# Optimization experiments

Measured on AMD Instinct MI355X. Metric: run time of the kernel, lower is better.

The kernel has to match this reference:

```python
import jax, jax.numpy as jnp
import numpy as np

B, N, A, M, D = 64, 128, 64, 128, 64  # batch, in_caps, in_dim, out_caps, out_dim
SCALE = 1.0 / np.sqrt(D).astype(np.float32)
W_INIT = np.sqrt(M / (A * N)).astype(np.float32)


def setup_inputs() -> dict:
    key = jax.random.key(0)
    k1, k2, k3, k4, k5 = jax.random.split(key, 5)
    return {
        "input": jax.random.normal(k1, (B, N, A), dtype=jnp.float32),
        "current_act": jax.random.uniform(k2, (B, N), dtype=jnp.float32),
        "next_capsule_value": jax.random.normal(k3, (B, M, D), dtype=jnp.float32),
        "next_act": jax.random.uniform(k4, (B, M), dtype=jnp.float32),
        "w": W_INIT * jax.random.normal(k5, (N, A, M, D), dtype=jnp.float32),
        "num_iter": 1,
    }


def reference(input, current_act, next_capsule_value, next_act, w, num_iter):
    # Per-(input-capsule, output-capsule) votes: bna,namd->bnmd (shared by both einsums)
    votes = jnp.einsum('bna,namd->bnmd', input, w)
    # Routing logits: agreement between votes and current output poses
    logits = jnp.einsum('bnmd,bmd->bnm', votes, next_capsule_value) * SCALE
    qk = jax.nn.softmax(logits, axis=2)
    # Modulate by next-layer activations and renormalize over output capsules
    qk = qk * next_act[:, None, :]
    qk = qk / (jnp.sum(qk, axis=2, keepdims=True) + 1e-10)
    # Weighted aggregation of votes, gated by input-capsule activations
    ncv = jnp.einsum('bnm,bnmd,bn->bmd', qk, votes, current_act)
    # act_type == 'ONES'; dropout rate 0.0 (identity); nonlinear_act is identity
    na = jnp.ones(ncv.shape[:2], dtype=ncv.dtype)
    return ncv, na, qk
```

## Files before the change

kernel.cpp:

```cpp
#include <hip/hip_runtime.h>

typedef __attribute__((ext_vector_type(8))) short bf16x8;
typedef __attribute__((ext_vector_type(4))) float f32x4;

constexpr int Bq = 64, Nq = 128, Aq = 64, Mq = 128, Dq = 64;
constexpr int MD = Mq * Dq;
constexpr int NM = Nq * Mq;
constexpr int NA = Nq * Aq;
constexpr int NCV_SZ = Bq * MD;
constexpr int NA_SZ  = Bq * Mq;
constexpr float SCALE = 0.125f;

__device__ __forceinline__ unsigned short f2b(float f) {
  unsigned u = __float_as_uint(f);
  return (unsigned short)((u + 0x7fffu + ((u >> 16) & 1u)) >> 16);
}
__device__ __forceinline__ unsigned cvt2(float lo, float hi) {
  return ((unsigned)f2b(hi) << 16) | (unsigned)f2b(lo);
}
__device__ __forceinline__ bf16x8 pack8(const float* v) {
  union { unsigned u[4]; bf16x8 b; } x;
  x.u[0] = cvt2(v[0], v[1]); x.u[1] = cvt2(v[2], v[3]);
  x.u[2] = cvt2(v[4], v[5]); x.u[3] = cvt2(v[6], v[7]);
  return x.b;
}
__device__ __forceinline__ void dma16(const float* g, float* l) {
  __builtin_amdgcn_global_load_lds(
      (const __attribute__((address_space(1))) unsigned*)g,
      (__attribute__((address_space(3))) unsigned*)l, 16, 0, 0);
}

__global__ __launch_bounds__(256) void k0_init(float* __restrict__ out) {
  int i = blockIdx.x * 256 + threadIdx.x;
  if (i < NCV_SZ) out[i] = 0.0f;
  else if (i < NCV_SZ + NA_SZ) out[i] = 1.0f;
}

__global__ __launch_bounds__(512, 4) void k1_logits(
    const float* __restrict__ input, const float* __restrict__ ncvin,
    const float* __restrict__ wgt, float* __restrict__ logits) {
  const int mc = blockIdx.x;
  const int n0 = blockIdx.y * 8;
  const int t = threadIdx.x;
  const int w8 = t >> 6, l = t & 63;
  const int wv_m = w8 & 3, wv_b = w8 >> 2;
  const int lr = l & 15, g = l >> 4;
  const int m = mc * 4 + wv_m;
  __shared__ float Wf[2][32 * 256];

  float cnv[2][4][4];
#pragma unroll
  for (int i = 0; i < 2; ++i)
#pragma unroll
    for (int j = 0; j < 4; ++j)
#pragma unroll
      for (int r = 0; r < 4; ++r)
        cnv[i][j][r] = ncvin[(size_t)(32 * wv_b + 16 * i + 4 * g + r) * MD + m * Dq + 16 * j + lr];

  auto stage = [&](int h) {
    const int hh = 15 - h;
    const int nn = n0 + (hh >> 1);
    const int ks = (hh & 1) * 32;
    float* dst = &Wf[h & 1][0];
#pragma unroll
    for (int rr = 0; rr < 4; ++rr) {
      const int al = w8 * 4 + rr;
      const char* gs = (const char*)(wgt + (size_t)(nn * Aq + ks + al) * MD + mc * 256)
                       + ((l * 16) ^ (((al >> 3) & 1) << 6));
      dma16((const float*)gs, dst + al * 256);
    }
  };
  stage(0);
  f32x4 acc[2][4];

  for (int h = 0; h < 16; ++h) {
    const int hh = 15 - h;
    const int nn = n0 + (hh >> 1);
    const int ks = (hh & 1) * 32;

    float av[2][8];
#pragma unroll
    for (int i = 0; i < 2; ++i) {
      const float* ap = input + (size_t)(32 * wv_b + 16 * i + lr) * NA + nn * Aq + ks + g * 8;
      *(float4*)&av[i][0] = *(const float4*)ap;
      *(float4*)&av[i][4] = *(const float4*)(ap + 4);
    }
    __builtin_amdgcn_sched_barrier(0);

    if (h < 15) {
      stage(h + 1);
      asm volatile("s_waitcnt vmcnt(4)" ::: "memory");
    } else {
      asm volatile("s_waitcnt vmcnt(0)" ::: "memory");
    }
    __builtin_amdgcn_s_barrier();

    if ((h & 1) == 0) {
#pragma unroll
      for (int i = 0; i < 2; ++i)
#pragma unroll
        for (int j = 0; j < 4; ++j) acc[i][j] = (f32x4)(0.0f);
    }

    bf16x8 af[2];
#pragma unroll
    for (int i = 0; i < 2; ++i) af[i] = pack8(av[i]);

    const float* bufp = &Wf[h & 1][0];
#pragma unroll
    for (int j = 0; j < 4; ++j) {
      const int cx = (64 * wv_m + 16 * j + lr) ^ ((g & 1) << 4);
      float bv[8];
#pragma unroll
      for (int e = 0; e < 8; ++e) bv[e] = bufp[(g * 8 + e) * 256 + cx];
      bf16x8 bf = pack8(bv);
#pragma unroll
      for (int i = 0; i < 2; ++i)
        acc[i][j] = __builtin_amdgcn_mfma_f32_16x16x32_bf16(af[i], bf, acc[i][j], 0, 0, 0);
    }
    __builtin_amdgcn_s_barrier();

    if (h & 1) {
      float lp[2][4];
#pragma unroll
      for (int i = 0; i < 2; ++i)
#pragma unroll
        for (int r = 0; r < 4; ++r) lp[i][r] = 0.0f;
#pragma unroll
      for (int i = 0; i < 2; ++i)
#pragma unroll
        for (int j = 0; j < 4; ++j)
#pragma unroll
          for (int r = 0; r < 4; ++r)
            lp[i][r] = fmaf(acc[i][j][r], cnv[i][j][r], lp[i][r]);
#pragma unroll
      for (int off = 1; off < 16; off <<= 1)
#pragma unroll
        for (int i = 0; i < 2; ++i)
#pragma unroll
          for (int r = 0; r < 4; ++r) lp[i][r] += __shfl_xor(lp[i][r], off);
      float ov = lp[0][0];
#pragma unroll
      for (int i = 0; i < 2; ++i)
#pragma unroll
        for (int r = 0; r < 4; ++r)
          ov = (lr == i * 4 + r) ? lp[i][r] : ov;
      if (lr < 8) {
        const int b = 32 * wv_b + 16 * (lr >> 2) + 4 * g + (lr & 3);
        logits[(size_t)b * NM + (size_t)nn * Mq + m] = SCALE * ov;
      }
    }
  }
}

__global__ __launch_bounds__(256) void k2_softmax(
    const float* __restrict__ next_act, float* __restrict__ qk) {
  const int row  = blockIdx.x * 4 + (threadIdx.x >> 6);
  const int lane = threadIdx.x & 63;
  const int b = row >> 7;
  float* p = qk + (size_t)row * Mq;
  float x0 = p[lane], x1 = p[lane + 64];
  float mx = fmaxf(x0, x1);
#pragma unroll
  for (int off = 32; off; off >>= 1) mx = fmaxf(mx, __shfl_xor(mx, off));
  float e0 = __expf(x0 - mx), e1 = __expf(x1 - mx);
  float s = e0 + e1;
#pragma unroll
  for (int off = 32; off; off >>= 1) s += __shfl_xor(s, off);
  float a0 = next_act[b * Mq + lane], a1 = next_act[b * Mq + lane + 64];
  float t0 = (e0 / s) * a0, t1 = (e1 / s) * a1;
  float s2 = t0 + t1;
#pragma unroll
  for (int off = 32; off; off >>= 1) s2 += __shfl_xor(s2, off);
  s2 += 1e-10f;
  p[lane]      = t0 / s2;
  p[lane + 64] = t1 / s2;
}

__global__ __launch_bounds__(512, 4) void k3_aggregate(
    const float* __restrict__ input, const float* __restrict__ cur_act,
    const float* __restrict__ wgt, const float* __restrict__ qk,
    float* __restrict__ ncv) {
  const int mc = blockIdx.x;
  const int n0 = blockIdx.y * 8;
  const int t = threadIdx.x;
  const int w8 = t >> 6, l = t & 63;
  const int wv_m = w8 & 3, wv_b = w8 >> 2;
  const int lr = l & 15, g = l >> 4;
  const int m = mc * 4 + wv_m;
  __shared__ float Wf[2][32 * 256];
  __shared__ float zl[8][4][64];

  {
    const int b = t >> 3, nn = t & 7;
    float4 q4 = *(const float4*)&qk[(size_t)b * NM + (size_t)(n0 + nn) * Mq + mc * 4];
    float ca = cur_act[b * Nq + n0 + nn];
    zl[nn][0][b] = q4.x * ca; zl[nn][1][b] = q4.y * ca;
    zl[nn][2][b] = q4.z * ca; zl[nn][3][b] = q4.w * ca;
  }
  __syncthreads();

  auto stage = [&](int h) {
    const int nn = n0 + (h >> 1);
    const int ks = (h & 1) * 32;
    float* dst = &Wf[h & 1][0];
#pragma unroll
    for (int rr = 0; rr < 4; ++rr) {
      const int al = w8 * 4 + rr;
      const char* gs = (const char*)(wgt + (size_t)(nn * Aq + ks + al) * MD + mc * 256)
                       + ((l * 16) ^ (((al >> 3) & 1) << 6));
      dma16((const float*)gs, dst + al * 256);
    }
  };
  stage(0);
  f32x4 acc[2][4];
#pragma unroll
  for (int i = 0; i < 2; ++i)
#pragma unroll
    for (int j = 0; j < 4; ++j) acc[i][j] = (f32x4)(0.0f);

  float zr[2];
  for (int h = 0; h < 16; ++h) {
    const int nnl = h >> 1;
    const int nn = n0 + nnl;
    const int ks = (h & 1) * 32;

    if ((h & 1) == 0) {
#pragma unroll
      for (int i = 0; i < 2; ++i) zr[i] = zl[nnl][wv_m][32 * wv_b + 16 * i + lr];
    }

    float av[2][8];
#pragma unroll
    for (int i = 0; i < 2; ++i) {
      const float* ap = input + (size_t)(32 * wv_b + 16 * i + lr) * NA + nn * Aq + ks + g * 8;
      *(float4*)&av[i][0] = *(const float4*)ap;
      *(float4*)&av[i][4] = *(const float4*)(ap + 4);
    }
    __builtin_amdgcn_sched_barrier(0);

    if (h < 15) {
      stage(h + 1);
      asm volatile("s_waitcnt vmcnt(4)" ::: "memory");
    } else {
      asm volatile("s_waitcnt vmcnt(0)" ::: "memory");
    }
    __builtin_amdgcn_s_barrier();

    bf16x8 af[2];
#pragma unroll
    for (int i = 0; i < 2; ++i) {
      float sv[8];
#pragma unroll
      for (int e = 0; e < 8; ++e) sv[e] = av[i][e] * zr[i];
      af[i] = pack8(sv);
    }

    const float* bufp = &Wf[h & 1][0];
#pragma unroll
    for (int j = 0; j < 4; ++j) {
      const int cx = (64 * wv_m + 16 * j + lr) ^ ((g & 1) << 4);
      float bv[8];
#pragma unroll
      for (int e = 0; e < 8; ++e) bv[e] = bufp[(g * 8 + e) * 256 + cx];
      bf16x8 bf = pack8(bv);
#pragma unroll
      for (int i = 0; i < 2; ++i)
        acc[i][j] = __builtin_amdgcn_mfma_f32_16x16x32_bf16(af[i], bf, acc[i][j], 0, 0, 0);
    }
    __builtin_amdgcn_s_barrier();
  }

#pragma unroll
  for (int i = 0; i < 2; ++i)
#pragma unroll
    for (int j = 0; j < 4; ++j) {
      const int d = 16 * j + lr;
#pragma unroll
      for (int r = 0; r < 4; ++r) {
        const int b = 32 * wv_b + 16 * i + 4 * g + r;
        atomicAdd(&ncv[(size_t)b * MD + m * Dq + d], acc[i][j][r]);
      }
    }
}

extern "C" void kernel_launch(void* const* d_in, const int* in_sizes, int n_in,
                              void* d_out, int out_size, void* d_ws, size_t ws_size,
                              hipStream_t stream) {
  const float* input    = (const float*)d_in[0];
  const float* cur_act  = (const float*)d_in[1];
  const float* ncvin    = (const float*)d_in[2];
  const float* next_act = (const float*)d_in[3];
  const float* wgt      = (const float*)d_in[4];

  float* out = (float*)d_out;
  float* ncv = out;
  float* qk  = out + NCV_SZ + NA_SZ;

  k0_init<<<(NCV_SZ + NA_SZ + 255) / 256, 256, 0, stream>>>(out);
  k1_logits<<<dim3(32, 16), 512, 0, stream>>>(input, ncvin, wgt, qk);
  k2_softmax<<<(Bq * Nq) / 4, 256, 0, stream>>>(next_act, qk);
  k3_aggregate<<<dim3(32, 16), 512, 0, stream>>>(input, cur_act, wgt, qk, ncv);
}
```

Baseline: 153.0 us.

## Deepen W staging to four LDS buffers and double per-block n range

Both GEMM kernels now handle 16 input capsules per block instead of 8, which halves the grid to 256 blocks and halves the atomic adds in the aggregate kernel. The W tile ring grows from two to four LDS buffers, with prefetch distance three, and the input-row register loads are double-buffered, so global loads are hidden behind MFMA work. The LDS footprint rises to 128KB per block and launch bounds drop to 2 blocks per CU, which lowers occupancy and may leave CUs underused with the smaller grid.

```diff
diff --git a/kernel.cpp b/kernel.cpp
--- a/kernel.cpp
+++ b/kernel.cpp
@@ -36,17 +36,17 @@
   else if (i < NCV_SZ + NA_SZ) out[i] = 1.0f;
 }
 
-__global__ __launch_bounds__(512, 4) void k1_logits(
+__global__ __launch_bounds__(512, 2) void k1_logits(
     const float* __restrict__ input, const float* __restrict__ ncvin,
     const float* __restrict__ wgt, float* __restrict__ logits) {
   const int mc = blockIdx.x;
-  const int n0 = blockIdx.y * 8;
+  const int n0 = blockIdx.y * 16;
   const int t = threadIdx.x;
   const int w8 = t >> 6, l = t & 63;
   const int wv_m = w8 & 3, wv_b = w8 >> 2;
   const int lr = l & 15, g = l >> 4;
   const int m = mc * 4 + wv_m;
-  __shared__ float Wf[2][32 * 256];
+  __shared__ float Wf[4][32 * 256];
 
   float cnv[2][4][4];
 #pragma unroll
@@ -57,11 +57,12 @@
       for (int r = 0; r < 4; ++r)
         cnv[i][j][r] = ncvin[(size_t)(32 * wv_b + 16 * i + 4 * g + r) * MD + m * Dq + 16 * j + lr];
 
-  auto stage = [&](int h) {
-    const int hh = 15 - h;
+  auto stageT = [&](int h) {
+    if (h > 31) return;
+    const int hh = 31 - h;
     const int nn = n0 + (hh >> 1);
     const int ks = (hh & 1) * 32;
-    float* dst = &Wf[h & 1][0];
+    float* dst = &Wf[h & 3][0];
 #pragma unroll
     for (int rr = 0; rr < 4; ++rr) {
       const int al = w8 * 4 + rr;
@@ -70,43 +71,23 @@
       dma16((const float*)gs, dst + al * 256);
     }
   };
-  stage(0);
-  f32x4 acc[2][4];
-
-  for (int h = 0; h < 16; ++h) {
-    const int hh = 15 - h;
+  auto loadAv = [&](int h, float (&av)[2][8]) {
+    if (h > 31) return;
+    const int hh = 31 - h;
     const int nn = n0 + (hh >> 1);
     const int ks = (hh & 1) * 32;
-
-    float av[2][8];
 #pragma unroll
     for (int i = 0; i < 2; ++i) {
       const float* ap = input + (size_t)(32 * wv_b + 16 * i + lr) * NA + nn * Aq + ks + g * 8;
       *(float4*)&av[i][0] = *(const float4*)ap;
       *(float4*)&av[i][4] = *(const float4*)(ap + 4);
     }
-    __builtin_amdgcn_sched_barrier(0);
-
-    if (h < 15) {
-      stage(h + 1);
-      asm volatile("s_waitcnt vmcnt(4)" ::: "memory");
-    } else {
-      asm volatile("s_waitcnt vmcnt(0)" ::: "memory");
-    }
-    __builtin_amdgcn_s_barrier();
-
-    if ((h & 1) == 0) {
-#pragma unroll
-      for (int i = 0; i < 2; ++i)
-#pragma unroll
-        for (int j = 0; j < 4; ++j) acc[i][j] = (f32x4)(0.0f);
-    }
-
+  };
+  auto mfmaPhase = [&](int h, float (&av)[2][8], f32x4 (&acc)[2][4]) {
     bf16x8 af[2];
 #pragma unroll
     for (int i = 0; i < 2; ++i) af[i] = pack8(av[i]);
-
-    const float* bufp = &Wf[h & 1][0];
+    const float* bufp = &Wf[h & 3][0];
 #pragma unroll
     for (int j = 0; j < 4; ++j) {
       const int cx = (64 * wv_m + 16 * j + lr) ^ ((g & 1) << 4);
@@ -118,9 +99,36 @@
       for (int i = 0; i < 2; ++i)
         acc[i][j] = __builtin_amdgcn_mfma_f32_16x16x32_bf16(af[i], bf, acc[i][j], 0, 0, 0);
     }
+  };
+
+  float avE[2][8], avO[2][8];
+  stageT(0);
+  loadAv(0, avE);
+  stageT(1);
+  stageT(2);
+
+  f32x4 acc[2][4];
+  for (int hp = 0; hp < 16; ++hp) {
+    const int h0 = hp * 2, h1 = h0 + 1;
+    if (hp == 0)      asm volatile("s_waitcnt vmcnt(8)" ::: "memory");
+    else if (hp < 15) asm volatile("s_waitcnt vmcnt(4)" ::: "memory");
+    else              asm volatile("s_waitcnt vmcnt(0)" ::: "memory");
     __builtin_amdgcn_s_barrier();
-
-    if (h & 1) {
+#pragma unroll
+    for (int i = 0; i < 2; ++i)
+#pragma unroll
+      for (int j = 0; j < 4; ++j) acc[i][j] = (f32x4)(0.0f);
+    mfmaPhase(h0, avE, acc);
+    __builtin_amdgcn_sched_barrier(0);
+    loadAv(h1, avO);
+    __builtin_amdgcn_sched_barrier(0);
+    stageT(h0 + 3);
+    if (hp < 15) asm volatile("s_waitcnt vmcnt(4)" ::: "memory");
+    else         asm volatile("s_waitcnt vmcnt(0)" ::: "memory");
+    __builtin_amdgcn_s_barrier();
+    mfmaPhase(h1, avO, acc);
+    {
+      const int nn = n0 + ((31 - h1) >> 1);
       float lp[2][4];
 #pragma unroll
       for (int i = 0; i < 2; ++i)
@@ -150,6 +158,10 @@
         logits[(size_t)b * NM + (size_t)nn * Mq + m] = SCALE * ov;
       }
     }
+    __builtin_amdgcn_sched_barrier(0);
+    loadAv(h0 + 2, avE);
+    __builtin_amdgcn_sched_barrier(0);
+    stageT(h1 + 3);
   }
 }
 
@@ -177,22 +189,24 @@
   p[lane + 64] = t1 / s2;
 }
 
-__global__ __launch_bounds__(512, 4) void k3_aggregate(
+__global__ __launch_bounds__(512, 2) void k3_aggregate(
     const float* __restrict__ input, const float* __restrict__ cur_act,
     const float* __restrict__ wgt, const float* __restrict__ qk,
     float* __restrict__ ncv) {
   const int mc = blockIdx.x;
-  const int n0 = blockIdx.y * 8;
+  const int n0 = blockIdx.y * 16;
   const int t = threadIdx.x;
   const int w8 = t >> 6, l = t & 63;
   const int wv_m = w8 & 3, wv_b = w8 >> 2;
   const int lr = l & 15, g = l >> 4;
   const int m = mc * 4 + wv_m;
-  __shared__ float Wf[2][32 * 256];
-  __shared__ float zl[8][4][64];
-
-  {
-    const int b = t >> 3, nn = t & 7;
+  __shared__ float Wf[4][32 * 256];
+  __shared__ float zl[16][4][64];
+
+#pragma unroll
+  for (int p = 0; p < 2; ++p) {
+    const int idx = t + p * 512;
+    const int b = idx >> 4, nn = idx & 15;
     float4 q4 = *(const float4*)&qk[(size_t)b * NM + (size_t)(n0 + nn) * Mq + mc * 4];
     float ca = cur_act[b * Nq + n0 + nn];
     zl[nn][0][b] = q4.x * ca; zl[nn][1][b] = q4.y * ca;
@@ -200,10 +214,11 @@
   }
   __syncthreads();
 
-  auto stage = [&](int h) {
+  auto stageT = [&](int h) {
+    if (h > 31) return;
     const int nn = n0 + (h >> 1);
     const int ks = (h & 1) * 32;
-    float* dst = &Wf[h & 1][0];
+    float* dst = &Wf[h & 3][0];
 #pragma unroll
     for (int rr = 0; rr < 4; ++rr) {
       const int al = w8 * 4 + rr;
@@ -212,41 +227,18 @@
       dma16((const float*)gs, dst + al * 256);
     }
   };
-  stage(0);
-  f32x4 acc[2][4];
-#pragma unroll
-  for (int i = 0; i < 2; ++i)
-#pragma unroll
-    for (int j = 0; j < 4; ++j) acc[i][j] = (f32x4)(0.0f);
-
-  float zr[2];
-  for (int h = 0; h < 16; ++h) {
-    const int nnl = h >> 1;
-    const int nn = n0 + nnl;
+  auto loadAv = [&](int h, float (&av)[2][8]) {
+    if (h > 31) return;
+    const int nn = n0 + (h >> 1);
     const int ks = (h & 1) * 32;
-
-    if ((h & 1) == 0) {
-#pragma unroll
-      for (int i = 0; i < 2; ++i) zr[i] = zl[nnl][wv_m][32 * wv_b + 16 * i + lr];
-    }
-
-    float av[2][8];
 #pragma unroll
     for (int i = 0; i < 2; ++i) {
       const float* ap = input + (size_t)(32 * wv_b + 16 * i + lr) * NA + nn * Aq + ks + g * 8;
       *(float4*)&av[i][0] = *(const float4*)ap;
       *(float4*)&av[i][4] = *(const float4*)(ap + 4);
     }
-    __builtin_amdgcn_sched_barrier(0);
-
-    if (h < 15) {
-      stage(h + 1);
-      asm volatile("s_waitcnt vmcnt(4)" ::: "memory");
-    } else {
-      asm volatile("s_waitcnt vmcnt(0)" ::: "memory");
-    }
-    __builtin_amdgcn_s_barrier();
-
+  };
+  auto mfmaPhase = [&](int h, float (&av)[2][8], float (&zr)[2], f32x4 (&acc)[2][4]) {
     bf16x8 af[2];
 #pragma unroll
     for (int i = 0; i < 2; ++i) {
@@ -255,8 +247,7 @@
       for (int e = 0; e < 8; ++e) sv[e] = av[i][e] * zr[i];
       af[i] = pack8(sv);
     }
-
-    const float* bufp = &Wf[h & 1][0];
+    const float* bufp = &Wf[h & 3][0];
 #pragma unroll
     for (int j = 0; j < 4; ++j) {
       const int cx = (64 * wv_m + 16 * j + lr) ^ ((g & 1) << 4);
@@ -268,7 +259,42 @@
       for (int i = 0; i < 2; ++i)
         acc[i][j] = __builtin_amdgcn_mfma_f32_16x16x32_bf16(af[i], bf, acc[i][j], 0, 0, 0);
     }
+  };
+
+  float avE[2][8], avO[2][8];
+  stageT(0);
+  loadAv(0, avE);
+  stageT(1);
+  stageT(2);
+
+  f32x4 acc[2][4];
+#pragma unroll
+  for (int i = 0; i < 2; ++i)
+#pragma unroll
+    for (int j = 0; j < 4; ++j) acc[i][j] = (f32x4)(0.0f);
+
+  float zr[2];
+  for (int hp = 0; hp < 16; ++hp) {
+    const int h0 = hp * 2, h1 = h0 + 1;
+    if (hp == 0)      asm volatile("s_waitcnt vmcnt(8)" ::: "memory");
+    else if (hp < 15) asm volatile("s_waitcnt vmcnt(4)" ::: "memory");
+    else              asm volatile("s_waitcnt vmcnt(0)" ::: "memory");
     __builtin_amdgcn_s_barrier();
+#pragma unroll
+    for (int i = 0; i < 2; ++i) zr[i] = zl[hp][wv_m][32 * wv_b + 16 * i + lr];
+    mfmaPhase(h0, avE, zr, acc);
+    __builtin_amdgcn_sched_barrier(0);
+    loadAv(h1, avO);
+    __builtin_amdgcn_sched_barrier(0);
+    stageT(h0 + 3);
+    if (hp < 15) asm volatile("s_waitcnt vmcnt(4)" ::: "memory");
+    else         asm volatile("s_waitcnt vmcnt(0)" ::: "memory");
+    __builtin_amdgcn_s_barrier();
+    mfmaPhase(h1, avO, zr, acc);
+    __builtin_amdgcn_sched_barrier(0);
+    loadAv(h0 + 2, avE);
+    __builtin_amdgcn_sched_barrier(0);
+    stageT(h1 + 3);
   }
 
 #pragma unroll
@@ -298,7 +324,7 @@
   float* qk  = out + NCV_SZ + NA_SZ;
 
   k0_init<<<(NCV_SZ + NA_SZ + 255) / 256, 256, 0, stream>>>(out);
-  k1_logits<<<dim3(32, 16), 512, 0, stream>>>(input, ncvin, wgt, qk);
+  k1_logits<<<dim3(32, 8), 512, 0, stream>>>(input, ncvin, wgt, qk);
   k2_softmax<<<(Bq * Nq) / 4, 256, 0, stream>>>(next_act, qk);
-  k3_aggregate<<<dim3(32, 16), 512, 0, stream>>>(input, cur_act, wgt, qk, ncv);
-}
+  k3_aggregate<<<dim3(32, 8), 512, 0, stream>>>(input, cur_act, wgt, qk, ncv);
+}
```

Result: slower. 161.0 us (+5.2%).
